# Performance work log

Measured on AMD Instinct MI355X. Metric: run time of the kernel, lower is better.

The kernel has to match this reference:

```python
import jax, jax.numpy as jnp
import numpy as np

SIGMA_LIST = [0.05, 0.1, 0.2]
WEIGHT_LIST = [0.3, 0.3, 0.4]


def setup_inputs() -> dict:
    key = jax.random.key(0)
    k1, k2, k3 = jax.random.split(key, 3)
    B, N, M, D, C = 1, 8192, 8192, 3, 16
    x = jax.random.uniform(k1, (B, N, D), dtype=jnp.float32)
    y = jax.random.uniform(k2, (B, M, D), dtype=jnp.float32)
    y_fea = jax.random.normal(k3, (B, M, C), dtype=jnp.float32)
    return {"x": x, "y": y, "y_fea": y_fea}


def reference(x, y, y_fea):
    x2 = jnp.sum(x * x, axis=-1)  # [B, N]
    y2 = jnp.sum(y * y, axis=-1)  # [B, M]
    xy = jnp.einsum("bnd,bmd->bnm", x, y)  # [B, N, M]
    d2 = jnp.maximum(x2[:, :, None] + y2[:, None, :] - 2.0 * xy, 0.0)
    out = jnp.zeros(x.shape[:2] + (y_fea.shape[-1],), dtype=y_fea.dtype)
    for sigma, w in zip(SIGMA_LIST, WEIGHT_LIST):
        k = jnp.exp(d2 * (-1.0 / (2.0 * sigma * sigma)))  # [B, N, M]
        k = k / jnp.sum(k, axis=-1, keepdims=True)  # row-normalize over neighbors
        out = out + w * jnp.einsum("bnm,bmc->bnc", k, y_fea)
    return out
```

## Files before the change

kernel.cpp:

```cpp
#include <hip/hip_runtime.h>


static constexpr int Nn = 8192;
static constexpr int Mm = 8192;
static constexpr int NCH = 8;
static constexpr int MC  = Mm / NCH;
static constexpr int NKT = MC / 32;
static constexpr float KC = 36.0673761f;
static constexpr float KD = -18.0336880f;

typedef _Float16 half8 __attribute__((ext_vector_type(8)));
typedef __fp16  fp16x2 __attribute__((ext_vector_type(2)));
typedef float  float4v __attribute__((ext_vector_type(4)));

#define MFMA_F16 __builtin_amdgcn_mfma_f32_16x16x32_f16
#define EXP2F(v) __builtin_amdgcn_exp2f(v)

__global__ __launch_bounds__(256) void mgsc_prep(
    const float* __restrict__ y, const float* __restrict__ yf,
    _Float16* __restrict__ fragy, _Float16* __restrict__ fragf)
{
    const int t = blockIdx.x * 256 + threadIdx.x;
    const int m = t >> 5, kk = t & 31;
    const float ax = y[3 * m], ay = y[3 * m + 1], az = y[3 * m + 2];
    const float Ycx = KC * ax, Ycy = KC * ay, Ycz = KC * az;
    const _Float16 Yhx = (_Float16)Ycx, Yhy = (_Float16)Ycy, Yhz = (_Float16)Ycz;
    const _Float16 Ylx = (_Float16)(Ycx - (float)Yhx);
    const _Float16 Yly = (_Float16)(Ycy - (float)Yhy);
    const _Float16 Ylz = (_Float16)(Ycz - (float)Yhz);
    const float Wy = KD * __fmaf_rn(ax, ax, __fmaf_rn(ay, ay, az * az));
    const _Float16 Wyh = (_Float16)Wy;
    const _Float16 Wyl = (_Float16)(Wy - (float)Wyh);
    _Float16 v = (_Float16)0.0f;
    switch (kk) {
        case 0: case 6: v = Yhx; break;
        case 1: case 7: v = Yhy; break;
        case 2: case 8: v = Yhz; break;
        case 3: v = Ylx; break;
        case 4: v = Yly; break;
        case 5: v = Ylz; break;
        case 9:  v = Wyh; break;
        case 10: v = Wyl; break;
        case 11: case 12: v = (_Float16)1.0f; break;
        default: break;
    }
    const int fragidx = ((m >> 5) << 1) + ((m >> 2) & 1);
    const int rho = (((m >> 3) & 3) << 2) + (m & 3);
    const int idx = (fragidx << 9) + ((((kk >> 3) << 4) + rho) << 3) + (kk & 7);
    fragy[idx] = v;
    if (t < Mm * 16) {
        const int m2 = t >> 4, c2 = t & 15;
        const int idx2 = ((m2 >> 5) << 9) + ((((m2 & 31) >> 3) << 4) + c2) * 8 + (m2 & 7);
        fragf[idx2] = (_Float16)yf[t];
    }
}

__global__ __launch_bounds__(256, 4) void mgsc_main(
    const float* __restrict__ x, const _Float16* __restrict__ fragy,
    const _Float16* __restrict__ fragf, float* __restrict__ part)
{
    const int tid  = threadIdx.x;
    const int wave = tid >> 6, lane = tid & 63;
    const int g    = lane >> 4, c = lane & 15;
    const int xb   = blockIdx.x, yb = blockIdx.y;
    const int n0   = (xb * 4 + wave) * 16;
    const int nrow = n0 + c;

    const float xx = x[3 * nrow], xy = x[3 * nrow + 1], xz = x[3 * nrow + 2];
    const _Float16 xhx = (_Float16)xx, xhy = (_Float16)xy, xhz = (_Float16)xz;
    const _Float16 xlx = (_Float16)(xx - (float)xhx);
    const _Float16 xly = (_Float16)(xy - (float)xhy);
    const _Float16 xlz = (_Float16)(xz - (float)xhz);
    const float Wx = KD * __fmaf_rn(xx, xx, __fmaf_rn(xy, xy, xz * xz));
    const _Float16 Wxh = (_Float16)Wx;
    const _Float16 Wxl = (_Float16)(Wx - (float)Wxh);
    const _Float16 z16 = (_Float16)0.0f, one16 = (_Float16)1.0f;
    half8 B1;
    if (g == 0)      B1 = half8{xhx, xhy, xhz, xhx, xhy, xhz, xlx, xly};
    else if (g == 1) B1 = half8{xlz, one16, one16, Wxh, Wxl, z16, z16, z16};
    else             B1 = half8{z16, z16, z16, z16, z16, z16, z16, z16};

    float4v acc0 = {0.f, 0.f, 0.f, 0.f}, acc1 = acc0, acc2 = acc0;
    float4v dac0 = acc0, dac1 = acc0, dac2 = acc0;
    const float4v z4 = acc0;

    const _Float16 bv = (c == 0) ? one16 : z16;
    half8 boneA = {bv, bv, bv, bv, bv, bv, bv, bv};

    const size_t ybase = (size_t)(yb * (MC / 16)) << 9;
    const size_t fbase = (size_t)(yb * NKT) << 9;

    for (int ktl = 0; ktl < NKT; ++ktl) {
        const half8 A1a = *reinterpret_cast<const half8*>(fragy + ybase + ((size_t)(2 * ktl) << 9) + (lane << 3));
        const half8 A1b = *reinterpret_cast<const half8*>(fragy + ybase + ((size_t)(2 * ktl + 1) << 9) + (lane << 3));
        const half8 Af  = *reinterpret_cast<const half8*>(fragf + fbase + ((size_t)ktl << 9) + (lane << 3));

        const float4v D1 = MFMA_F16(A1a, B1, z4, 0, 0, 0);
        const float4v D2 = MFMA_F16(A1b, B1, z4, 0, 0, 0);

        union { fp16x2 h2[4]; half8 v; } E2p, E1p, E0p;
        E2p.h2[0] = __builtin_amdgcn_cvt_pkrtz(EXP2F(D1[0]), EXP2F(D1[1]));
        E2p.h2[1] = __builtin_amdgcn_cvt_pkrtz(EXP2F(D1[2]), EXP2F(D1[3]));
        E2p.h2[2] = __builtin_amdgcn_cvt_pkrtz(EXP2F(D2[0]), EXP2F(D2[1]));
        E2p.h2[3] = __builtin_amdgcn_cvt_pkrtz(EXP2F(D2[2]), EXP2F(D2[3]));
#pragma unroll
        for (int jj = 0; jj < 4; ++jj) {
            const fp16x2 s2 = E2p.h2[jj] * E2p.h2[jj];
            E1p.h2[jj] = s2 * s2;
            const fp16x2 s1 = E1p.h2[jj] * E1p.h2[jj];
            E0p.h2[jj] = s1 * s1;
        }
        acc0 = MFMA_F16(Af, E0p.v, acc0, 0, 0, 0);
        acc1 = MFMA_F16(Af, E1p.v, acc1, 0, 0, 0);
        acc2 = MFMA_F16(Af, E2p.v, acc2, 0, 0, 0);
        dac0 = MFMA_F16(boneA, E0p.v, dac0, 0, 0, 0);
        dac1 = MFMA_F16(boneA, E1p.v, dac1, 0, 0, 0);
        dac2 = MFMA_F16(boneA, E2p.v, dac2, 0, 0, 0);
    }

    float* row = part + ((size_t)yb * Nn + (n0 + c)) * 52;
    *reinterpret_cast<float4v*>(row + 4 * g)      = acc0;
    *reinterpret_cast<float4v*>(row + 16 + 4 * g) = acc1;
    *reinterpret_cast<float4v*>(row + 32 + 4 * g) = acc2;
    if (g == 0) {
        row[48] = dac0[0];
        row[49] = dac1[0];
        row[50] = dac2[0];
    }
}

__global__ __launch_bounds__(256) void mgsc_reduce(
    const float* __restrict__ part, float* __restrict__ out)
{
    const int t = blockIdx.x * 256 + threadIdx.x;
    const int n = t >> 4, c = t & 15;
    float s0 = 0.f, s1 = 0.f, s2 = 0.f, d0 = 0.f, d1 = 0.f, d2 = 0.f;
#pragma unroll
    for (int k = 0; k < NCH; ++k) {
        const float* row = part + ((size_t)k * Nn + n) * 52;
        s0 += row[c];
        s1 += row[16 + c];
        s2 += row[32 + c];
        d0 += row[48];
        d1 += row[49];
        d2 += row[50];
    }
    out[(size_t)n * 16 + c] = 0.3f * s0 / d0 + 0.3f * s1 / d1 + 0.4f * s2 / d2;
}

__global__ __launch_bounds__(256) void mgsc_fused(
    const float* __restrict__ x, const float* __restrict__ y,
    const float* __restrict__ yf, float* __restrict__ out)
{
    __shared__ float yS[256 * 3];
    __shared__ float yfS[256 * 16];
    const int tid = threadIdx.x;
    const int n   = blockIdx.x * 256 + tid;
    const float xx = x[3 * n], xy = x[3 * n + 1], xz = x[3 * n + 2];
    float a0[16], a1[16], a2[16];
#pragma unroll
    for (int c = 0; c < 16; ++c) { a0[c] = 0.f; a1[c] = 0.f; a2[c] = 0.f; }
    float den0 = 0.f, den1 = 0.f, den2 = 0.f;
    for (int mt = 0; mt < Mm; mt += 256) {
        const float4* ysrc = reinterpret_cast<const float4*>(y + (size_t)mt * 3);
        if (tid < 192) reinterpret_cast<float4*>(yS)[tid] = ysrc[tid];
        const float4* fsrc = reinterpret_cast<const float4*>(yf + (size_t)mt * 16);
#pragma unroll
        for (int k = 0; k < 4; ++k)
            reinterpret_cast<float4*>(yfS)[tid + 256 * k] = fsrc[tid + 256 * k];
        __syncthreads();
        for (int mm = 0; mm < 256; ++mm) {
            const float dx = xx - yS[3 * mm], dy = xy - yS[3 * mm + 1], dz = xz - yS[3 * mm + 2];
            const float d2 = dx * dx + dy * dy + dz * dz;
            const float e2 = __expf(-12.5f * d2);
            const float t = e2 * e2, e1 = t * t, u = e1 * e1, e0 = u * u;
            den0 += e0; den1 += e1; den2 += e2;
            const float4* fr = reinterpret_cast<const float4*>(yfS + mm * 16);
#pragma unroll
            for (int k = 0; k < 4; ++k) {
                const float4 f = fr[k];
                a0[4*k+0] += e0 * f.x; a0[4*k+1] += e0 * f.y; a0[4*k+2] += e0 * f.z; a0[4*k+3] += e0 * f.w;
                a1[4*k+0] += e1 * f.x; a1[4*k+1] += e1 * f.y; a1[4*k+2] += e1 * f.z; a1[4*k+3] += e1 * f.w;
                a2[4*k+0] += e2 * f.x; a2[4*k+1] += e2 * f.y; a2[4*k+2] += e2 * f.z; a2[4*k+3] += e2 * f.w;
            }
        }
        __syncthreads();
    }
    const float r0 = 0.3f / den0, r1 = 0.3f / den1, r2 = 0.4f / den2;
#pragma unroll
    for (int c = 0; c < 16; ++c)
        out[(size_t)n * 16 + c] = a0[c] * r0 + a1[c] * r1 + a2[c] * r2;
}

extern "C" void kernel_launch(void* const* d_in, const int* in_sizes, int n_in,
                              void* d_out, int out_size, void* d_ws, size_t ws_size,
                              hipStream_t stream) {
    const float* x  = (const float*)d_in[0];
    const float* y  = (const float*)d_in[1];
    const float* yf = (const float*)d_in[2];
    float* out = (float*)d_out;

    const size_t fragyB = (size_t)(Mm / 16) * 512 * sizeof(_Float16);
    const size_t fragfB = (size_t)Mm * 16 * sizeof(_Float16);
    const size_t partB  = (size_t)NCH * Nn * 52 * sizeof(float);
    if (fragyB + fragfB + partB > ws_size) {
        mgsc_fused<<<Nn / 256, 256, 0, stream>>>(x, y, yf, out);
        return;
    }
    _Float16* fragy = (_Float16*)d_ws;
    _Float16* fragf = (_Float16*)((char*)d_ws + fragyB);
    float*    part  = (float*)((char*)d_ws + fragyB + fragfB);

    mgsc_prep<<<(Mm * 32) / 256, 256, 0, stream>>>(y, yf, fragy, fragf);
    mgsc_main<<<dim3(Nn / 64, NCH), 256, 0, stream>>>(x, fragy, fragf, part);
    mgsc_reduce<<<(Nn * 16) / 256, 256, 0, stream>>>(part, out);
}
```

Baseline: 85.57 us.

## Fuse split-M reduction into main kernel via LDS across eight waves

Each block now handles 16 query rows with 8 waves, each wave covering one M chunk, and the per-chunk partial numerators and denominators are reduced in shared memory inside the same kernel. This removes the global partial buffer, its write and read traffic, and the separate reduce kernel launch. In exchange the grid becomes 512 blocks of 512 threads, all waves must synchronize before the reduction, and only half the threads do the final combine.

```diff
diff --git a/kernel.cpp b/kernel.cpp
--- a/kernel.cpp
+++ b/kernel.cpp
@@ -55,15 +55,17 @@
     }
 }
 
-__global__ __launch_bounds__(256, 4) void mgsc_main(
+__global__ __launch_bounds__(512, 4) void mgsc_main(
     const float* __restrict__ x, const _Float16* __restrict__ fragy,
-    const _Float16* __restrict__ fragf, float* __restrict__ part)
+    const _Float16* __restrict__ fragf, float* __restrict__ out)
 {
+    __shared__ float ldsN[NCH][16][52];
+    __shared__ float ldsD[NCH][16][3];
+
     const int tid  = threadIdx.x;
-    const int wave = tid >> 6, lane = tid & 63;
+    const int w    = tid >> 6, lane = tid & 63;
     const int g    = lane >> 4, c = lane & 15;
-    const int xb   = blockIdx.x, yb = blockIdx.y;
-    const int n0   = (xb * 4 + wave) * 16;
+    const int n0   = blockIdx.x * 16;
     const int nrow = n0 + c;
 
     const float xx = x[3 * nrow], xy = x[3 * nrow + 1], xz = x[3 * nrow + 2];
@@ -87,8 +89,8 @@
     const _Float16 bv = (c == 0) ? one16 : z16;
     half8 boneA = {bv, bv, bv, bv, bv, bv, bv, bv};
 
-    const size_t ybase = (size_t)(yb * (MC / 16)) << 9;
-    const size_t fbase = (size_t)(yb * NKT) << 9;
+    const size_t ybase = (size_t)(w * (MC / 16)) << 9;
+    const size_t fbase = (size_t)(w * NKT) << 9;
 
     for (int ktl = 0; ktl < NKT; ++ktl) {
         const half8 A1a = *reinterpret_cast<const half8*>(fragy + ybase + ((size_t)(2 * ktl) << 9) + (lane << 3));
@@ -118,34 +120,33 @@
         dac2 = MFMA_F16(boneA, E2p.v, dac2, 0, 0, 0);
     }
 
-    float* row = part + ((size_t)yb * Nn + (n0 + c)) * 52;
-    *reinterpret_cast<float4v*>(row + 4 * g)      = acc0;
-    *reinterpret_cast<float4v*>(row + 16 + 4 * g) = acc1;
-    *reinterpret_cast<float4v*>(row + 32 + 4 * g) = acc2;
-    if (g == 0) {
-        row[48] = dac0[0];
-        row[49] = dac1[0];
-        row[50] = dac2[0];
-    }
-}
-
-__global__ __launch_bounds__(256) void mgsc_reduce(
-    const float* __restrict__ part, float* __restrict__ out)
-{
-    const int t = blockIdx.x * 256 + threadIdx.x;
-    const int n = t >> 4, c = t & 15;
-    float s0 = 0.f, s1 = 0.f, s2 = 0.f, d0 = 0.f, d1 = 0.f, d2 = 0.f;
-#pragma unroll
-    for (int k = 0; k < NCH; ++k) {
-        const float* row = part + ((size_t)k * Nn + n) * 52;
-        s0 += row[c];
-        s1 += row[16 + c];
-        s2 += row[32 + c];
-        d0 += row[48];
-        d1 += row[49];
-        d2 += row[50];
-    }
-    out[(size_t)n * 16 + c] = 0.3f * s0 / d0 + 0.3f * s1 / d1 + 0.4f * s2 / d2;
+    {
+        float* rowp = &ldsN[w][c][0];
+        *reinterpret_cast<float4v*>(rowp + 4 * g)      = acc0;
+        *reinterpret_cast<float4v*>(rowp + 16 + 4 * g) = acc1;
+        *reinterpret_cast<float4v*>(rowp + 32 + 4 * g) = acc2;
+        if (g == 0) {
+            ldsD[w][c][0] = dac0[0];
+            ldsD[w][c][1] = dac1[0];
+            ldsD[w][c][2] = dac2[0];
+        }
+    }
+    __syncthreads();
+
+    if (tid < 256) {
+        const int nl = tid >> 4, co = tid & 15;
+        float s0 = 0.f, s1 = 0.f, s2 = 0.f, d0 = 0.f, d1 = 0.f, d2 = 0.f;
+#pragma unroll
+        for (int k = 0; k < NCH; ++k) {
+            s0 += ldsN[k][nl][co];
+            s1 += ldsN[k][nl][16 + co];
+            s2 += ldsN[k][nl][32 + co];
+            d0 += ldsD[k][nl][0];
+            d1 += ldsD[k][nl][1];
+            d2 += ldsD[k][nl][2];
+        }
+        out[(size_t)(n0 + nl) * 16 + co] = 0.3f * s0 / d0 + 0.3f * s1 / d1 + 0.4f * s2 / d2;
+    }
 }
 
 __global__ __launch_bounds__(256) void mgsc_fused(
@@ -202,16 +203,13 @@
 
     const size_t fragyB = (size_t)(Mm / 16) * 512 * sizeof(_Float16);
     const size_t fragfB = (size_t)Mm * 16 * sizeof(_Float16);
-    const size_t partB  = (size_t)NCH * Nn * 52 * sizeof(float);
-    if (fragyB + fragfB + partB > ws_size) {
+    if (fragyB + fragfB > ws_size) {
         mgsc_fused<<<Nn / 256, 256, 0, stream>>>(x, y, yf, out);
         return;
     }
     _Float16* fragy = (_Float16*)d_ws;
     _Float16* fragf = (_Float16*)((char*)d_ws + fragyB);
-    float*    part  = (float*)((char*)d_ws + fragyB + fragfB);
 
     mgsc_prep<<<(Mm * 32) / 256, 256, 0, stream>>>(y, yf, fragy, fragf);
-    mgsc_main<<<dim3(Nn / 64, NCH), 256, 0, stream>>>(x, fragy, fragf, part);
-    mgsc_reduce<<<(Nn * 16) / 256, 256, 0, stream>>>(part, out);
-}
+    mgsc_main<<<Nn / 16, 512, 0, stream>>>(x, fragy, fragf, out);
+}
```

Measured after the change: 82.11 us. -4.0%, faster.
